# Performance work log

Hardware: AMD Instinct MI355X
Metric: run time of the kernel (lower is better)

The kernel has to match this reference:

```python
import jax, jax.numpy as jnp
import numpy as np
import math

B, LS, N = 32, 512, 32          # batch, seq-of-sets length, concepts per set
V, D = 50000, 128               # num_emb, emb_dim
H = D // 2                      # attention hidden dim (emb_dim // 2)


def setup_inputs() -> dict:
    key = jax.random.key(0)
    ks = jax.random.split(key, 10)
    input_ids = jax.random.randint(ks[0], (B, LS, N), 0, V)
    id_mask = (jax.random.uniform(ks[1], (B, LS, N)) > 0.3).astype(jnp.float32)
    input_times = jax.random.uniform(ks[2], (B, LS), dtype=jnp.float32)
    emb_table = jax.random.normal(ks[3], (V, D), dtype=jnp.float32) * 0.02
    qW = jax.random.normal(ks[4], (H, D), dtype=jnp.float32) * 0.05
    qb = jnp.zeros((H,), jnp.float32)
    kW = jax.random.normal(ks[5], (H, D), dtype=jnp.float32) * 0.05
    kb = jnp.zeros((H,), jnp.float32)
    theta_table = jax.random.normal(ks[6], (V, 1), dtype=jnp.float32) * 0.1
    mu_table = jax.random.normal(ks[7], (V, 1), dtype=jnp.float32) * 0.1
    return {"input_ids": input_ids, "id_mask": id_mask, "input_times": input_times,
            "emb_table": emb_table, "qW": qW, "qb": qb, "kW": kW, "kb": kb,
            "theta_table": theta_table, "mu_table": mu_table}


def reference(input_ids, id_mask, input_times, emb_table, qW, qb, kW, kb, theta_table, mu_table):
    bs, ls, n = input_ids.shape
    ids = input_ids.reshape(bs * ls, n)            # (BL, n)
    mask = id_mask.reshape(bs * ls, n)             # (BL, n)
    times = input_times.reshape(bs * ls)           # (BL,)

    x = emb_table[ids]                             # (BL, n, D)  (dropout = identity in eval)

    # ScaledDotAttn (faithful, including the bmm-based mask outer product)
    q = jnp.einsum('bnd,hd->bnh', x, qW) + qb      # (BL, n, H)
    k = jnp.einsum('bnd,hd->bnh', x, kW) + kb      # (BL, n, H)
    m = jnp.where(mask[:, :, None] > 0.5, 0.0, -1000000000.0)   # (BL, n, 1)
    kmask = m * jnp.swapaxes(m, -1, -2)            # (BL, n, n) == bmm(m, m^T)
    scores = jnp.einsum('bnh,bmh->bnm', q, k) / math.sqrt(H) + kmask
    attn = jax.nn.softmax(scores, axis=-1)
    out = jnp.einsum('bnm,bmd->bnd', attn, x)      # (BL, n, D)

    # time_discount pooling
    theta = theta_table[ids][..., 0]               # (BL, n)
    mu = mu_table[ids][..., 0]                     # (BL, n)
    sx = jax.nn.sigmoid(theta - mu * times[:, None])   # (BL, n)
    pooled = jnp.sum(out * (sx * mask)[:, :, None], axis=1)  # (BL, D)
    return pooled.reshape(bs, ls, D)
```

## Files before the change

### kernel.cpp

```cpp
#include <hip/hip_runtime.h>

typedef __attribute__((ext_vector_type(4))) float  f32x4;
typedef __attribute__((ext_vector_type(8))) short  s16x8;
typedef __attribute__((ext_vector_type(4))) short  s16x4;

#define V_NUM   50000

__device__ __forceinline__ short f2bf(float f) {
  unsigned u = __float_as_uint(f);
  u += 0x7FFFu + ((u >> 16) & 1u);
  return (short)(u >> 16);
}
__device__ __forceinline__ float bf2f(short s) {
  return __uint_as_float(((unsigned)(unsigned short)s) << 16);
}


__global__ __launch_bounds__(256) void prep_mt_kernel(
    const float* __restrict__ qW, const float* __restrict__ kW,
    unsigned short* __restrict__ MTg)
{
  const int idx = blockIdx.x * 256 + threadIdx.x;
  const int e = idx >> 7, d = idx & 127;
  float acc = 0.f;
#pragma unroll 8
  for (int h = 0; h < 64; ++h) acc += qW[h * 128 + d] * kW[h * 128 + e];
  MTg[idx] = (unsigned short)f2bf(0.125f * acc);
}

__global__ __launch_bounds__(256) void prep_z_kernel(
    const float* __restrict__ emb, const unsigned short* __restrict__ MTg,
    unsigned short* __restrict__ tab)
{
  __shared__ __attribute__((aligned(16))) unsigned short shMT[128 * 136];
  for (int i = threadIdx.x; i < 2048; i += 256) {
    const int row = i >> 4, c = (i & 15) * 8;
    *reinterpret_cast<s16x8*>(&shMT[row * 136 + c]) =
        *(const s16x8*)(MTg + row * 128 + c);
  }
  __syncthreads();

  const int wave = threadIdx.x >> 6;
  const int lane = threadIdx.x & 63;
  const int lr = lane & 15;
  const int q4 = lane >> 4;
  const int v0 = (blockIdx.x * 4 + wave) * 16;
  if (v0 >= V_NUM) return;
  const int r = v0 + lr;

  s16x8 xf[4];
#pragma unroll
  for (int s = 0; s < 4; ++s) {
    const float* p = emb + (size_t)r * 128 + 8 * q4 + 32 * s;
    f32x4 a = *(const f32x4*)p;
    f32x4 b = *(const f32x4*)(p + 4);
    s16x8 o;
#pragma unroll
    for (int e = 0; e < 4; ++e) { o[e] = f2bf(a[e]); o[4 + e] = f2bf(b[e]); }
    xf[s] = o;
    *reinterpret_cast<s16x8*>(tab + (size_t)r * 256 + 8 * q4 + 32 * s) = o;
  }

#pragma unroll
  for (int nbl = 0; nbl < 8; ++nbl) {
    f32x4 ya = {0.f, 0.f, 0.f, 0.f};
#pragma unroll
    for (int kd = 0; kd < 4; ++kd) {
      const s16x8 mtf = *reinterpret_cast<const s16x8*>(
          &shMT[(16 * nbl + lr) * 136 + 32 * kd + 8 * q4]);
      ya = __builtin_amdgcn_mfma_f32_16x16x32_bf16(mtf, xf[kd], ya, 0, 0, 0);
    }
    s16x4 zo;
#pragma unroll
    for (int rg = 0; rg < 4; ++rg) zo[rg] = f2bf(ya[rg]);
    *reinterpret_cast<s16x4*>(
        tab + (size_t)r * 256 + 128 + 16 * nbl + 4 * q4) = zo;
  }
}

__global__ __launch_bounds__(256, 4) void concept_main_kernel(
    const int* __restrict__ ids_g, const float* __restrict__ mask_g,
    const float* __restrict__ times_g, const unsigned short* __restrict__ tab,
    const float* __restrict__ theta_t, const float* __restrict__ mu_t,
    float* __restrict__ out)
{
  __shared__ float sh_c[4][32];
  __shared__ int   sh_id[4][32];

  const int wave = threadIdx.x >> 6;
  const int lane = threadIdx.x & 63;
  const int set  = blockIdx.x * 4 + wave;
  const int lr = lane & 15;
  const int q4 = lane >> 4;

  const int* sids = ids_g + (size_t)set * 32;
  const float t = times_g[set];

  const int id0 = sids[lr];
  const int id1 = sids[lr + 16];
  if (lane < 32) sh_id[wave][lane] = sids[lane];

  const float m0 = mask_g[(size_t)set * 32 + lr];
  const float m1 = mask_g[(size_t)set * 32 + lr + 16];
  const float w0 = m0 / (1.f + __expf(mu_t[id0] * t - theta_t[id0]));
  const float w1 = m1 / (1.f + __expf(mu_t[id1] * t - theta_t[id1]));

  s16x8 xf[2][4], zf[2][4];
  {
    const unsigned short* p0 = tab + (size_t)id0 * 256 + 8 * q4;
    const unsigned short* p1 = tab + (size_t)id1 * 256 + 8 * q4;
#pragma unroll
    for (int s = 0; s < 4; ++s) {
      xf[0][s] = *(const s16x8*)(p0 + 32 * s);
      xf[1][s] = *(const s16x8*)(p1 + 32 * s);
      zf[0][s] = *(const s16x8*)(p0 + 128 + 32 * s);
      zf[1][s] = *(const s16x8*)(p1 + 128 + 32 * s);
    }
  }

  f32x4 acc[2][2];
#pragma unroll
  for (int jb = 0; jb < 2; ++jb)
#pragma unroll
    for (int ib = 0; ib < 2; ++ib) acc[jb][ib] = f32x4{0.f, 0.f, 0.f, 0.f};

#pragma unroll
  for (int s = 0; s < 4; ++s)
#pragma unroll
    for (int ib = 0; ib < 2; ++ib)
#pragma unroll
      for (int jb = 0; jb < 2; ++jb)
        acc[jb][ib] = __builtin_amdgcn_mfma_f32_16x16x32_bf16(
            xf[jb][s], zf[ib][s], acc[jb][ib], 0, 0, 0);

  float cc[2][4] = {{0.f,0.f,0.f,0.f},{0.f,0.f,0.f,0.f}};
#pragma unroll
  for (int ib = 0; ib < 2; ++ib) {
    float mx = -3.0e38f;
#pragma unroll
    for (int jb = 0; jb < 2; ++jb)
#pragma unroll
      for (int r = 0; r < 4; ++r) mx = fmaxf(mx, acc[jb][ib][r]);
    mx = fmaxf(mx, __shfl_xor(mx, 16));
    mx = fmaxf(mx, __shfl_xor(mx, 32));
    float p[2][4], sum = 0.f;
#pragma unroll
    for (int jb = 0; jb < 2; ++jb)
#pragma unroll
      for (int r = 0; r < 4; ++r) {
        p[jb][r] = __expf(acc[jb][ib][r] - mx);
        sum += p[jb][r];
      }
    sum += __shfl_xor(sum, 16);
    sum += __shfl_xor(sum, 32);
    const float rs = (ib ? w1 : w0) / sum;
#pragma unroll
    for (int jb = 0; jb < 2; ++jb)
#pragma unroll
      for (int r = 0; r < 4; ++r) cc[jb][r] += rs * p[jb][r];
  }

#pragma unroll
  for (int off = 1; off <= 8; off <<= 1)
#pragma unroll
    for (int jb = 0; jb < 2; ++jb)
#pragma unroll
      for (int r = 0; r < 4; ++r) cc[jb][r] += __shfl_xor(cc[jb][r], off);

  if (lr == 0) {
#pragma unroll
    for (int jb = 0; jb < 2; ++jb)
#pragma unroll
      for (int r = 0; r < 4; ++r) sh_c[wave][16 * jb + 4 * q4 + r] = cc[jb][r];
  }
  __syncthreads();

  float pa[8] = {0.f,0.f,0.f,0.f,0.f,0.f,0.f,0.f};
#pragma unroll
  for (int t8 = 0; t8 < 8; ++t8) {
    const int j = 4 * t8 + q4;
    const int idj = sh_id[wave][j];
    const float cj = sh_c[wave][j];
    const s16x8 xv = *(const s16x8*)(tab + (size_t)idj * 256 + 8 * lr);
#pragma unroll
    for (int e = 0; e < 8; ++e) pa[e] += cj * bf2f(xv[e]);
  }
#pragma unroll
  for (int e = 0; e < 8; ++e) {
    pa[e] += __shfl_xor(pa[e], 16);
    pa[e] += __shfl_xor(pa[e], 32);
  }
  if (q4 == 0) {
    float* op = out + (size_t)set * 128 + 8 * lr;
    f32x4 o0 = {pa[0], pa[1], pa[2], pa[3]};
    f32x4 o1 = {pa[4], pa[5], pa[6], pa[7]};
    *(f32x4*)op       = o0;
    *(f32x4*)(op + 4) = o1;
  }
}

extern "C" void kernel_launch(void* const* d_in, const int* in_sizes, int n_in,
                              void* d_out, int out_size, void* d_ws, size_t ws_size,
                              hipStream_t stream) {
  const int*   ids   = (const int*)  d_in[0];
  const float* mask  = (const float*)d_in[1];
  const float* times = (const float*)d_in[2];
  const float* emb   = (const float*)d_in[3];
  const float* qW    = (const float*)d_in[4];
  const float* kW    = (const float*)d_in[6];
  const float* theta = (const float*)d_in[8];
  const float* mu    = (const float*)d_in[9];
  float* out = (float*)d_out;

  char* ws = (char*)d_ws;
  unsigned short* tab = (unsigned short*)(ws);
  unsigned short* MTg = (unsigned short*)(ws + 25600000);

  prep_mt_kernel<<<64, 256, 0, stream>>>(qW, kW, MTg);
  prep_z_kernel<<<782, 256, 0, stream>>>(emb, MTg, tab);
  concept_main_kernel<<<4096, 256, 0, stream>>>(ids, mask, times, tab,
                                                theta, mu, out);
}
```

Measured before the change: 150.8 us.

## Precompute per-token q/k projections in fp8 and use fp8 MFMA for scores

Replaces the folded qW^T·kW matrix approach with per-vocabulary q and k projections, each quantized to e4m3 fp8 with a scale of 64, packed into a 384-byte record next to the bf16 embedding. The main kernel now gathers 32 fp8 bytes per token instead of 512 bytes of bf16 x and z. It computes scores with fp8 MFMA and rescales inside the softmax exp. This also merges the two prep kernels into one and raises the occupancy hint to 8. It cuts gather bandwidth and MFMA work at the cost of fp8 accuracy in the attention scores.

```diff
diff --git a/kernel.cpp b/kernel.cpp
--- a/kernel.cpp
+++ b/kernel.cpp
@@ -2,9 +2,9 @@
 
 typedef __attribute__((ext_vector_type(4))) float  f32x4;
 typedef __attribute__((ext_vector_type(8))) short  s16x8;
-typedef __attribute__((ext_vector_type(4))) short  s16x4;
-
-#define V_NUM   50000
+typedef __attribute__((ext_vector_type(2))) long   i64x2;
+
+#define V_NUM 50000
 
 __device__ __forceinline__ short f2bf(float f) {
   unsigned u = __float_as_uint(f);
@@ -15,28 +15,43 @@
   return __uint_as_float(((unsigned)(unsigned short)s) << 16);
 }
 
-
-__global__ __launch_bounds__(256) void prep_mt_kernel(
-    const float* __restrict__ qW, const float* __restrict__ kW,
-    unsigned short* __restrict__ MTg)
+__device__ __forceinline__ unsigned f2e4m3(float x) {
+  float a = fabsf(x);
+  unsigned sgn = (__float_as_uint(x) >> 24) & 0x80u;
+  if (a > 448.f) a = 448.f;
+  if (a < 0.015625f) {
+    int m = (int)rintf(a * 512.f);
+    return sgn | (unsigned)m;
+  }
+  unsigned u = __float_as_uint(a);
+  unsigned lsb = (u >> 20) & 1u;
+  u += 0x0007FFFFu + lsb;
+  int E = (int)(u >> 23) - 127;
+  unsigned code = ((unsigned)(E + 7) << 3) | ((u >> 20) & 7u);
+  if (code > 0x7Eu) code = 0x7Eu;
+  return sgn | code;
+}
+
+__global__ __launch_bounds__(256) void prep_tab_kernel(
+    const float* __restrict__ emb, const float* __restrict__ qW,
+    const float* __restrict__ kW, unsigned char* __restrict__ tab)
 {
-  const int idx = blockIdx.x * 256 + threadIdx.x;
-  const int e = idx >> 7, d = idx & 127;
-  float acc = 0.f;
-#pragma unroll 8
-  for (int h = 0; h < 64; ++h) acc += qW[h * 128 + d] * kW[h * 128 + e];
-  MTg[idx] = (unsigned short)f2bf(0.125f * acc);
-}
-
-__global__ __launch_bounds__(256) void prep_z_kernel(
-    const float* __restrict__ emb, const unsigned short* __restrict__ MTg,
-    unsigned short* __restrict__ tab)
-{
-  __shared__ __attribute__((aligned(16))) unsigned short shMT[128 * 136];
-  for (int i = threadIdx.x; i < 2048; i += 256) {
+  __shared__ __attribute__((aligned(16))) unsigned short shQ[64 * 136];
+  __shared__ __attribute__((aligned(16))) unsigned short shK[64 * 136];
+
+  for (int i = threadIdx.x; i < 1024; i += 256) {
     const int row = i >> 4, c = (i & 15) * 8;
-    *reinterpret_cast<s16x8*>(&shMT[row * 136 + c]) =
-        *(const s16x8*)(MTg + row * 128 + c);
+    f32x4 a = *(const f32x4*)(qW + row * 128 + c);
+    f32x4 b = *(const f32x4*)(qW + row * 128 + c + 4);
+    s16x8 o;
+#pragma unroll
+    for (int e = 0; e < 4; ++e) { o[e] = f2bf(a[e]); o[4 + e] = f2bf(b[e]); }
+    *reinterpret_cast<s16x8*>(&shQ[row * 136 + c]) = o;
+    a = *(const f32x4*)(kW + row * 128 + c);
+    b = *(const f32x4*)(kW + row * 128 + c + 4);
+#pragma unroll
+    for (int e = 0; e < 4; ++e) { o[e] = f2bf(a[e]); o[4 + e] = f2bf(b[e]); }
+    *reinterpret_cast<s16x8*>(&shK[row * 136 + c]) = o;
   }
   __syncthreads();
 
@@ -47,40 +62,47 @@
   const int v0 = (blockIdx.x * 4 + wave) * 16;
   if (v0 >= V_NUM) return;
   const int r = v0 + lr;
+  unsigned char* rec = tab + (size_t)r * 384;
 
   s16x8 xf[4];
 #pragma unroll
-  for (int s = 0; s < 4; ++s) {
-    const float* p = emb + (size_t)r * 128 + 8 * q4 + 32 * s;
+  for (int kd = 0; kd < 4; ++kd) {
+    const float* p = emb + (size_t)r * 128 + 32 * kd + 8 * q4;
     f32x4 a = *(const f32x4*)p;
     f32x4 b = *(const f32x4*)(p + 4);
     s16x8 o;
 #pragma unroll
     for (int e = 0; e < 4; ++e) { o[e] = f2bf(a[e]); o[4 + e] = f2bf(b[e]); }
-    xf[s] = o;
-    *reinterpret_cast<s16x8*>(tab + (size_t)r * 256 + 8 * q4 + 32 * s) = o;
-  }
-
-#pragma unroll
-  for (int nbl = 0; nbl < 8; ++nbl) {
-    f32x4 ya = {0.f, 0.f, 0.f, 0.f};
-#pragma unroll
-    for (int kd = 0; kd < 4; ++kd) {
-      const s16x8 mtf = *reinterpret_cast<const s16x8*>(
-          &shMT[(16 * nbl + lr) * 136 + 32 * kd + 8 * q4]);
-      ya = __builtin_amdgcn_mfma_f32_16x16x32_bf16(mtf, xf[kd], ya, 0, 0, 0);
+    xf[kd] = o;
+    *reinterpret_cast<s16x8*>(rec + 64 * kd + 16 * q4) = o;
+  }
+
+#pragma unroll
+  for (int tgt = 0; tgt < 2; ++tgt) {
+    const unsigned short* W = tgt ? shK : shQ;
+#pragma unroll
+    for (int nbl = 0; nbl < 4; ++nbl) {
+      f32x4 a = {0.f, 0.f, 0.f, 0.f};
+#pragma unroll
+      for (int kd = 0; kd < 4; ++kd) {
+        const s16x8 wf = *reinterpret_cast<const s16x8*>(
+            &W[(16 * nbl + lr) * 136 + 32 * kd + 8 * q4]);
+        a = __builtin_amdgcn_mfma_f32_16x16x32_bf16(wf, xf[kd], a, 0, 0, 0);
+      }
+      unsigned pk =  f2e4m3(a[0] * 64.f)
+                  | (f2e4m3(a[1] * 64.f) << 8)
+                  | (f2e4m3(a[2] * 64.f) << 16)
+                  | (f2e4m3(a[3] * 64.f) << 24);
+      const int pos = 32 * (2 * (nbl & 1) + (q4 >> 1)) + 8 * (nbl >> 1)
+                    + 4 * (q4 & 1);
+      *reinterpret_cast<unsigned*>(rec + 256 + 16 * tgt + pos) = pk;
     }
-    s16x4 zo;
-#pragma unroll
-    for (int rg = 0; rg < 4; ++rg) zo[rg] = f2bf(ya[rg]);
-    *reinterpret_cast<s16x4*>(
-        tab + (size_t)r * 256 + 128 + 16 * nbl + 4 * q4) = zo;
-  }
-}
-
-__global__ __launch_bounds__(256, 4) void concept_main_kernel(
+  }
+}
+
+__global__ __launch_bounds__(256, 8) void concept_main_kernel(
     const int* __restrict__ ids_g, const float* __restrict__ mask_g,
-    const float* __restrict__ times_g, const unsigned short* __restrict__ tab,
+    const float* __restrict__ times_g, const unsigned char* __restrict__ tab,
     const float* __restrict__ theta_t, const float* __restrict__ mu_t,
     float* __restrict__ out)
 {
@@ -105,18 +127,12 @@
   const float w0 = m0 / (1.f + __expf(mu_t[id0] * t - theta_t[id0]));
   const float w1 = m1 / (1.f + __expf(mu_t[id1] * t - theta_t[id1]));
 
-  s16x8 xf[2][4], zf[2][4];
-  {
-    const unsigned short* p0 = tab + (size_t)id0 * 256 + 8 * q4;
-    const unsigned short* p1 = tab + (size_t)id1 * 256 + 8 * q4;
-#pragma unroll
-    for (int s = 0; s < 4; ++s) {
-      xf[0][s] = *(const s16x8*)(p0 + 32 * s);
-      xf[1][s] = *(const s16x8*)(p1 + 32 * s);
-      zf[0][s] = *(const s16x8*)(p0 + 128 + 32 * s);
-      zf[1][s] = *(const s16x8*)(p1 + 128 + 32 * s);
-    }
-  }
+  const unsigned char* r0 = tab + (size_t)id0 * 384 + 256 + 32 * q4;
+  const unsigned char* r1 = tab + (size_t)id1 * 384 + 256 + 32 * q4;
+  const i64x2 qv0 = *(const i64x2*)(r0);
+  const i64x2 kv0 = *(const i64x2*)(r0 + 16);
+  const i64x2 qv1 = *(const i64x2*)(r1);
+  const i64x2 kv1 = *(const i64x2*)(r1 + 16);
 
   f32x4 acc[2][2];
 #pragma unroll
@@ -125,13 +141,18 @@
     for (int ib = 0; ib < 2; ++ib) acc[jb][ib] = f32x4{0.f, 0.f, 0.f, 0.f};
 
 #pragma unroll
-  for (int s = 0; s < 4; ++s)
+  for (int s = 0; s < 2; ++s) {
+    const long qa[2] = {qv0[s], qv1[s]};
+    const long ka[2] = {kv0[s], kv1[s]};
 #pragma unroll
     for (int ib = 0; ib < 2; ++ib)
 #pragma unroll
       for (int jb = 0; jb < 2; ++jb)
-        acc[jb][ib] = __builtin_amdgcn_mfma_f32_16x16x32_bf16(
-            xf[jb][s], zf[ib][s], acc[jb][ib], 0, 0, 0);
+        acc[jb][ib] = __builtin_amdgcn_mfma_f32_16x16x32_fp8_fp8(
+            ka[jb], qa[ib], acc[jb][ib], 0, 0, 0);
+  }
+
+  const float SC = 3.0517578125e-05f;
 
   float cc[2][4] = {{0.f,0.f,0.f,0.f},{0.f,0.f,0.f,0.f}};
 #pragma unroll
@@ -148,7 +169,7 @@
     for (int jb = 0; jb < 2; ++jb)
 #pragma unroll
       for (int r = 0; r < 4; ++r) {
-        p[jb][r] = __expf(acc[jb][ib][r] - mx);
+        p[jb][r] = __expf((acc[jb][ib][r] - mx) * SC);
         sum += p[jb][r];
       }
     sum += __shfl_xor(sum, 16);
@@ -181,7 +202,7 @@
     const int j = 4 * t8 + q4;
     const int idj = sh_id[wave][j];
     const float cj = sh_c[wave][j];
-    const s16x8 xv = *(const s16x8*)(tab + (size_t)idj * 256 + 8 * lr);
+    const s16x8 xv = *(const s16x8*)(tab + (size_t)idj * 384 + lr * 16);
 #pragma unroll
     for (int e = 0; e < 8; ++e) pa[e] += cj * bf2f(xv[e]);
   }
@@ -212,12 +233,9 @@
   const float* mu    = (const float*)d_in[9];
   float* out = (float*)d_out;
 
-  char* ws = (char*)d_ws;
-  unsigned short* tab = (unsigned short*)(ws);
-  unsigned short* MTg = (unsigned short*)(ws + 25600000);
-
-  prep_mt_kernel<<<64, 256, 0, stream>>>(qW, kW, MTg);
-  prep_z_kernel<<<782, 256, 0, stream>>>(emb, MTg, tab);
+  unsigned char* tab = (unsigned char*)d_ws;
+
+  prep_tab_kernel<<<782, 256, 0, stream>>>(emb, qW, kW, tab);
   concept_main_kernel<<<4096, 256, 0, stream>>>(ids, mask, times, tab,
                                                 theta, mu, out);
 }
```

Result: faster. 126.6 us (-16.0%).
